# Kernel optimization log

Measured on AMD Instinct MI355X. Metric: run time of the kernel, lower is better.

Reference implementation:

```python
import jax, jax.numpy as jnp
import numpy as np

FEATURE_DIM = 512
NUM_HEADS = 8
HEAD_DIM = FEATURE_DIM // NUM_HEADS
B, L = 4, 2048


def setup_inputs() -> dict:
    key = jax.random.key(0)
    ks = jax.random.split(key, 10)
    s = 1.0 / np.sqrt(FEATURE_DIM)
    inp = {
        "ppg": jax.random.normal(ks[0], (B, FEATURE_DIM, L), dtype=jnp.float32),
        "ecg": jax.random.normal(ks[1], (B, FEATURE_DIM, L), dtype=jnp.float32),
        "Wq": jax.random.uniform(ks[2], (FEATURE_DIM, FEATURE_DIM), jnp.float32, -s, s),
        "bq": jnp.zeros((FEATURE_DIM,), jnp.float32),
        "Wk": jax.random.uniform(ks[3], (FEATURE_DIM, FEATURE_DIM), jnp.float32, -s, s),
        "bk": jnp.zeros((FEATURE_DIM,), jnp.float32),
        "Wv": jax.random.uniform(ks[4], (FEATURE_DIM, FEATURE_DIM), jnp.float32, -s, s),
        "bv": jnp.zeros((FEATURE_DIM,), jnp.float32),
        "Wo": jax.random.uniform(ks[5], (FEATURE_DIM, FEATURE_DIM), jnp.float32, -s, s),
        "bo": jnp.zeros((FEATURE_DIM,), jnp.float32),
    }
    return inp


def reference(ppg, ecg, Wq, bq, Wk, bk, Wv, bv, Wo, bo):
    # ppg/ecg: (B, C, L) -> (B, L, C)
    x = jnp.transpose(ppg, (0, 2, 1))
    y = jnp.transpose(ecg, (0, 2, 1))
    q = x @ Wq.T + bq  # (B, L, C)
    k = y @ Wk.T + bk
    v = y @ Wv.T + bv
    # split heads: (B, H, L, D)
    def split(t):
        return jnp.transpose(t.reshape(B, L, NUM_HEADS, HEAD_DIM), (0, 2, 1, 3))
    qh, kh, vh = split(q), split(k), split(v)
    scores = jnp.einsum('bhqd,bhkd->bhqk', qh, kh) / jnp.sqrt(jnp.float32(HEAD_DIM))
    probs = jax.nn.softmax(scores, axis=-1)  # dropout is identity in eval mode
    ctx = jnp.einsum('bhqk,bhkd->bhqd', probs, vh)
    ctx = jnp.transpose(ctx, (0, 2, 1, 3)).reshape(B, L, FEATURE_DIM)
    out = ctx @ Wo.T + bo + x  # residual with transposed ppg
    return jnp.transpose(out, (0, 2, 1))  # (B, C, L)
```

## Files before the change

kernel.cpp:

```cpp
#include <hip/hip_runtime.h>
#include <hip/hip_bf16.h>

static constexpr int Bc = 4;
static constexpr int Lc = 2048;
static constexpr int Cc = 512;
static constexpr int Hc = 8;
static constexpr int Dc = 64;

using short8  = __attribute__((ext_vector_type(8))) short;
using float4v = __attribute__((ext_vector_type(4))) float;

static __device__ __forceinline__ unsigned short f2bf(float f) {
    __hip_bfloat16 h = __float2bfloat16(f);
    return *reinterpret_cast<unsigned short*>(&h);
}

__global__ __launch_bounds__(256) void prep_kernel(
    const float* __restrict__ ppg, const float* __restrict__ ecg,
    const float* __restrict__ Wq, const float* __restrict__ Wk,
    const float* __restrict__ Wv, const float* __restrict__ Wo,
    unsigned short* __restrict__ Xt_ppg, unsigned short* __restrict__ Xt_ecg,
    unsigned short* __restrict__ Wbf)
{
    __shared__ float Ts[64 * 69];
    const int task = blockIdx.x;
    const int tid  = threadIdx.x;

    if (task < 2048) {
        const int src = task >> 10;
        const int rem = task & 1023;
        const int b   = rem >> 8;
        const int c0  = ((rem >> 5) & 7) * 64;
        const int l0  = (rem & 31) * 64;
        const float* X = src ? ecg : ppg;
        unsigned short* Xt = src ? Xt_ecg : Xt_ppg;

        #pragma unroll
        for (int j = 0; j < 4; ++j) {
            int idx = tid + j * 256;
            int c = idx >> 4, l4 = idx & 15;
            float4 v = *(const float4*)(X + ((size_t)b * Cc + c0 + c) * Lc + l0 + l4 * 4);
            Ts[c * 69 + l4 * 4 + 0] = v.x;
            Ts[c * 69 + l4 * 4 + 1] = v.y;
            Ts[c * 69 + l4 * 4 + 2] = v.z;
            Ts[c * 69 + l4 * 4 + 3] = v.w;
        }
        __syncthreads();
        #pragma unroll
        for (int j = 0; j < 8; ++j) {
            int u = tid + j * 256;
            int l = u >> 5, p2 = u & 31;
            float a = Ts[(2 * p2) * 69 + l];
            float bb = Ts[(2 * p2 + 1) * 69 + l];
            ushort2 pk; pk.x = f2bf(a); pk.y = f2bf(bb);
            *(ushort2*)(Xt + ((size_t)b * Lc + l0 + l) * Cc + c0 + 2 * p2) = pk;
        }
    } else {
        const int wb   = task - 2048;
        const int widx = wb >> 7;
        const float* W = widx == 0 ? Wq : widx == 1 ? Wk : widx == 2 ? Wv : Wo;
        size_t off = (size_t)(wb & 127) * 2048 + (size_t)tid * 8;
        float4 v0 = *(const float4*)(W + off);
        float4 v1 = *(const float4*)(W + off + 4);
        unsigned short pk[8] = {f2bf(v0.x), f2bf(v0.y), f2bf(v0.z), f2bf(v0.w),
                                f2bf(v1.x), f2bf(v1.y), f2bf(v1.z), f2bf(v1.w)};
        *(short8*)(Wbf + (size_t)widx * Cc * Cc + off) = *(const short8*)pk;
    }
}

__global__ __launch_bounds__(256) void proj_kernel(
    const unsigned short* __restrict__ Xt_ppg,
    const unsigned short* __restrict__ Xt_ecg,
    const unsigned short* __restrict__ Wbf,
    const float* __restrict__ bq, const float* __restrict__ bk,
    const float* __restrict__ bv,
    unsigned short* __restrict__ Qw, unsigned short* __restrict__ Kw,
    unsigned short* __restrict__ Vtw)
{
    constexpr int LDW = 72;
    const int z = blockIdx.z, p = z >> 2, b = z & 3;
    const int l0 = blockIdx.x * 64, n0 = blockIdx.y * 64;
    const unsigned short* X = (p == 0) ? Xt_ppg : Xt_ecg;
    const unsigned short* W = Wbf + (size_t)p * Cc * Cc;
    const float* bias = (p == 0) ? bq : (p == 1) ? bk : bv;

    const int tid = threadIdx.x, wave = tid >> 6, lane = tid & 63;
    const int l16 = lane & 15, quad = lane >> 4;

    __shared__ __align__(16) unsigned short At[64 * LDW];
    __shared__ __align__(16) unsigned short Bt[64 * LDW];

    float4v acc[4] = {};

    for (int c0 = 0; c0 < Cc; c0 += 64) {
        #pragma unroll
        for (int j = 0; j < 2; ++j) {
            int e = tid + j * 256;
            int row = e >> 3, c8 = e & 7;
            *(short8*)&At[row * LDW + c8 * 8] =
                *(const short8*)(X + ((size_t)b * Lc + l0 + row) * Cc + c0 + c8 * 8);
            *(short8*)&Bt[row * LDW + c8 * 8] =
                *(const short8*)(W + (size_t)(n0 + row) * Cc + c0 + c8 * 8);
        }
        __syncthreads();

        if (p < 2) {
            #pragma unroll
            for (int ks = 0; ks < 2; ++ks) {
                short8 af = *(const short8*)&At[(wave * 16 + l16) * LDW + ks * 32 + quad * 8];
                #pragma unroll
                for (int t = 0; t < 4; ++t) {
                    short8 bf = *(const short8*)&Bt[(t * 16 + l16) * LDW + ks * 32 + quad * 8];
                    acc[t] = __builtin_amdgcn_mfma_f32_16x16x32_bf16(af, bf, acc[t], 0, 0, 0);
                }
            }
        } else {
            #pragma unroll
            for (int ks = 0; ks < 2; ++ks) {
                short8 af = *(const short8*)&Bt[(wave * 16 + l16) * LDW + ks * 32 + quad * 8];
                #pragma unroll
                for (int t = 0; t < 4; ++t) {
                    short8 bf = *(const short8*)&At[(t * 16 + l16) * LDW + ks * 32 + quad * 8];
                    acc[t] = __builtin_amdgcn_mfma_f32_16x16x32_bf16(af, bf, acc[t], 0, 0, 0);
                }
            }
        }
        __syncthreads();
    }

    const int h = n0 >> 6;
    const int bh = b * Hc + h;

    if (p < 2) {
        const float sc = (p == 0) ? 0.18033688011112042f : 1.0f;
        unsigned short* dst = (p == 0) ? Qw : Kw;
        #pragma unroll
        for (int t = 0; t < 4; ++t) {
            float bia = bias[n0 + t * 16 + l16];
            #pragma unroll
            for (int r = 0; r < 4; ++r) {
                int l = l0 + wave * 16 + quad * 4 + r;
                dst[((size_t)bh * Lc + l) * Dc + t * 16 + l16] =
                    f2bf((acc[t][r] + bia) * sc);
            }
        }
    } else {
        #pragma unroll
        for (int t = 0; t < 4; ++t) {
            #pragma unroll
            for (int r = 0; r < 4; ++r) {
                int d = wave * 16 + quad * 4 + r;
                float bia = bias[n0 + d];
                int l = l0 + t * 16 + l16;
                Vtw[((size_t)bh * Dc + d) * Lc + l] = f2bf(acc[t][r] + bia);
            }
        }
    }
}

__global__ __launch_bounds__(256) void attn_mfma_kernel(
    const unsigned short* __restrict__ Qg,
    const unsigned short* __restrict__ Kg,
    const unsigned short* __restrict__ Vtg,
    unsigned short* __restrict__ ctx)
{
    constexpr int LDW = 72;
    const int bh   = blockIdx.y;
    const int q0   = blockIdx.x * 128;
    const int tid  = threadIdx.x;
    const int wave = tid >> 6;
    const int lane = tid & 63;
    const int l16  = lane & 15;
    const int quad = lane >> 4;

    __shared__ __align__(16) unsigned short Kt[64 * LDW];
    __shared__ __align__(16) unsigned short Vt[64 * LDW];
    __shared__ __align__(16) unsigned short PT[128 * LDW];

    const unsigned short* Qb = Qg + ((size_t)bh * Lc + q0) * Dc;
    #pragma unroll
    for (int j = 0; j < 4; ++j) {
        int e = tid + j * 256;
        int row = e >> 3, c8 = e & 7;
        *(short8*)&PT[row * LDW + c8 * 8] =
            *(const short8*)(Qb + row * Dc + c8 * 8);
    }
    __syncthreads();

    short8 qf[2][2];
    #pragma unroll
    for (int qt = 0; qt < 2; ++qt)
        #pragma unroll
        for (int ks = 0; ks < 2; ++ks)
            qf[qt][ks] = *(const short8*)&PT[(wave * 32 + qt * 16 + l16) * LDW
                                             + ks * 32 + quad * 8];

    float4v O[4][2] = {};
    float lsum[2] = {0.0f, 0.0f};

    for (int kc = 0; kc < Lc; kc += 64) {
        __syncthreads();
        const unsigned short* Kb = Kg + ((size_t)bh * Lc + kc) * Dc;
        const unsigned short* Vb = Vtg + (size_t)bh * (Dc * Lc) + kc;
        #pragma unroll
        for (int j = 0; j < 2; ++j) {
            int e = tid + j * 256;
            int row = e >> 3, c8 = e & 7;
            *(short8*)&Kt[row * LDW + c8 * 8] =
                *(const short8*)(Kb + row * Dc + c8 * 8);
            *(short8*)&Vt[row * LDW + c8 * 8] =
                *(const short8*)(Vb + (size_t)row * Lc + c8 * 8);
        }
        __syncthreads();

        float4v S[4][2];
        #pragma unroll
        for (int kt = 0; kt < 4; ++kt)
            #pragma unroll
            for (int qt = 0; qt < 2; ++qt)
                S[kt][qt] = (float4v){0.f, 0.f, 0.f, 0.f};
        #pragma unroll
        for (int ks = 0; ks < 2; ++ks) {
            #pragma unroll
            for (int kt = 0; kt < 4; ++kt) {
                short8 af = *(const short8*)&Kt[(kt * 16 + l16) * LDW
                                                + ks * 32 + quad * 8];
                #pragma unroll
                for (int qt = 0; qt < 2; ++qt)
                    S[kt][qt] = __builtin_amdgcn_mfma_f32_16x16x32_bf16(
                        af, qf[qt][ks], S[kt][qt], 0, 0, 0);
            }
        }

        #pragma unroll
        for (int qt = 0; qt < 2; ++qt) {
            float ls = 0.0f;
            #pragma unroll
            for (int kt = 0; kt < 4; ++kt) {
                float p0 = __builtin_amdgcn_exp2f(S[kt][qt][0]);
                float p1 = __builtin_amdgcn_exp2f(S[kt][qt][1]);
                float p2 = __builtin_amdgcn_exp2f(S[kt][qt][2]);
                float p3 = __builtin_amdgcn_exp2f(S[kt][qt][3]);
                ls += (p0 + p1) + (p2 + p3);
                ushort4 pk;
                pk.x = f2bf(p0); pk.y = f2bf(p1); pk.z = f2bf(p2); pk.w = f2bf(p3);
                *(ushort4*)&PT[(wave * 32 + qt * 16 + l16) * LDW
                               + kt * 16 + quad * 4] = pk;
            }
            lsum[qt] += ls;
        }

        #pragma unroll
        for (int ks = 0; ks < 2; ++ks) {
            short8 pf[2];
            #pragma unroll
            for (int qt = 0; qt < 2; ++qt)
                pf[qt] = *(const short8*)&PT[(wave * 32 + qt * 16 + l16) * LDW
                                             + ks * 32 + quad * 8];
            #pragma unroll
            for (int dt = 0; dt < 4; ++dt) {
                short8 vf = *(const short8*)&Vt[(dt * 16 + l16) * LDW
                                                + ks * 32 + quad * 8];
                #pragma unroll
                for (int qt = 0; qt < 2; ++qt)
                    O[dt][qt] = __builtin_amdgcn_mfma_f32_16x16x32_bf16(
                        vf, pf[qt], O[dt][qt], 0, 0, 0);
            }
        }
    }

    float inv_l[2];
    #pragma unroll
    for (int qt = 0; qt < 2; ++qt) {
        float t = lsum[qt];
        t += __shfl_xor(t, 16, 64);
        t += __shfl_xor(t, 32, 64);
        inv_l[qt] = 1.0f / t;
    }
    const int b = bh >> 3, h = bh & 7;
    #pragma unroll
    for (int dt = 0; dt < 4; ++dt) {
        #pragma unroll
        for (int qt = 0; qt < 2; ++qt) {
            int q = q0 + wave * 32 + qt * 16 + l16;
            ushort4 pk;
            pk.x = f2bf(O[dt][qt][0] * inv_l[qt]);
            pk.y = f2bf(O[dt][qt][1] * inv_l[qt]);
            pk.z = f2bf(O[dt][qt][2] * inv_l[qt]);
            pk.w = f2bf(O[dt][qt][3] * inv_l[qt]);
            *(ushort4*)(ctx + ((size_t)b * Lc + q) * Cc
                        + h * Dc + dt * 16 + quad * 4) = pk;
        }
    }
}

__global__ __launch_bounds__(256) void outproj_kernel(
    const unsigned short* __restrict__ ctx, const unsigned short* __restrict__ Wo_bf,
    const float* __restrict__ bo, const float* __restrict__ ppg,
    float* __restrict__ out)
{
    constexpr int LDW = 72;
    const int b = blockIdx.z;
    const int l0 = blockIdx.x * 64, n0 = blockIdx.y * 64;
    const int tid = threadIdx.x, wave = tid >> 6, lane = tid & 63;
    const int l16 = lane & 15, quad = lane >> 4;

    __shared__ __align__(16) unsigned short At[64 * LDW];
    __shared__ __align__(16) unsigned short Bt[64 * LDW];

    float4v acc[4] = {};

    for (int c0 = 0; c0 < Cc; c0 += 64) {
        #pragma unroll
        for (int j = 0; j < 2; ++j) {
            int e = tid + j * 256;
            int row = e >> 3, c8 = e & 7;
            *(short8*)&At[row * LDW + c8 * 8] =
                *(const short8*)(Wo_bf + (size_t)(n0 + row) * Cc + c0 + c8 * 8);
            *(short8*)&Bt[row * LDW + c8 * 8] =
                *(const short8*)(ctx + ((size_t)b * Lc + l0 + row) * Cc + c0 + c8 * 8);
        }
        __syncthreads();

        #pragma unroll
        for (int ks = 0; ks < 2; ++ks) {
            short8 af = *(const short8*)&At[(wave * 16 + l16) * LDW + ks * 32 + quad * 8];
            #pragma unroll
            for (int t = 0; t < 4; ++t) {
                short8 bf = *(const short8*)&Bt[(t * 16 + l16) * LDW + ks * 32 + quad * 8];
                acc[t] = __builtin_amdgcn_mfma_f32_16x16x32_bf16(af, bf, acc[t], 0, 0, 0);
            }
        }
        __syncthreads();
    }

    #pragma unroll
    for (int t = 0; t < 4; ++t) {
        #pragma unroll
        for (int r = 0; r < 4; ++r) {
            int n = n0 + wave * 16 + quad * 4 + r;
            int l = l0 + t * 16 + l16;
            size_t oidx = ((size_t)b * Cc + n) * Lc + l;
            out[oidx] = acc[t][r] + bo[n] + ppg[oidx];
        }
    }
}

extern "C" void kernel_launch(void* const* d_in, const int* in_sizes, int n_in,
                              void* d_out, int out_size, void* d_ws, size_t ws_size,
                              hipStream_t stream) {
    const float* ppg = (const float*)d_in[0];
    const float* ecg = (const float*)d_in[1];
    const float* Wq  = (const float*)d_in[2];
    const float* bq  = (const float*)d_in[3];
    const float* Wk  = (const float*)d_in[4];
    const float* bk  = (const float*)d_in[5];
    const float* Wv  = (const float*)d_in[6];
    const float* bv  = (const float*)d_in[7];
    const float* Wo  = (const float*)d_in[8];
    const float* bo  = (const float*)d_in[9];
    float* out = (float*)d_out;

    const size_t plane = (size_t)Bc * Lc * Cc;
    unsigned short* Xt_ppg = (unsigned short*)d_ws;
    unsigned short* Xt_ecg = Xt_ppg + plane;
    unsigned short* Wbf    = Xt_ecg + plane;
    unsigned short* Qw     = Wbf + (size_t)4 * Cc * Cc;
    unsigned short* Kw     = Qw + plane;
    unsigned short* Vtw    = Kw + plane;
    unsigned short* ctx    = Vtw + plane;

    prep_kernel<<<2560, 256, 0, stream>>>(ppg, ecg, Wq, Wk, Wv, Wo,
                                          Xt_ppg, Xt_ecg, Wbf);

    dim3 g1(Lc / 64, Cc / 64, 3 * Bc);
    proj_kernel<<<g1, 256, 0, stream>>>(Xt_ppg, Xt_ecg, Wbf, bq, bk, bv,
                                        Qw, Kw, Vtw);

    dim3 g2(Lc / 128, Bc * Hc);
    attn_mfma_kernel<<<g2, 256, 0, stream>>>(Qw, Kw, Vtw, ctx);

    dim3 g3(Lc / 64, Cc / 64, Bc);
    outproj_kernel<<<g3, 256, 0, stream>>>(ctx, Wbf + (size_t)3 * Cc * Cc,
                                           bo, ppg, out);
}
```

Baseline: 211.4 us.

## Register-prefetch next tiles in projection and attention, retile both kernels

Both the projection GEMM and the attention kernel now load the next K-chunk (or K/V tile) from global memory into registers while the current tile is being consumed from shared memory, overlapping load latency with MFMA work. The projection kernel doubles its L tile to 128 rows, so each block reuses the weight tile across more rows. The attention kernel halves its query tile to 64 rows, giving twice as many blocks for more occupancy and parallelism, at the cost of re-reading K/V more often. Register pressure rises, and an extra barrier per iteration is added in attention.

```diff
diff --git a/kernel.cpp b/kernel.cpp
--- a/kernel.cpp
+++ b/kernel.cpp
@@ -79,7 +79,7 @@
 {
     constexpr int LDW = 72;
     const int z = blockIdx.z, p = z >> 2, b = z & 3;
-    const int l0 = blockIdx.x * 64, n0 = blockIdx.y * 64;
+    const int l0 = blockIdx.x * 128, n0 = blockIdx.y * 64;
     const unsigned short* X = (p == 0) ? Xt_ppg : Xt_ecg;
     const unsigned short* W = Wbf + (size_t)p * Cc * Cc;
     const float* bias = (p == 0) ? bq : (p == 1) ? bk : bv;
@@ -87,41 +87,67 @@
     const int tid = threadIdx.x, wave = tid >> 6, lane = tid & 63;
     const int l16 = lane & 15, quad = lane >> 4;
 
-    __shared__ __align__(16) unsigned short At[64 * LDW];
+    __shared__ __align__(16) unsigned short At[128 * LDW];
     __shared__ __align__(16) unsigned short Bt[64 * LDW];
 
-    float4v acc[4] = {};
+    float4v acc[8] = {};
+    short8 areg[4], breg[2];
+
+    const int arow = tid >> 3, ac8 = tid & 7;
+    #pragma unroll
+    for (int j = 0; j < 4; ++j)
+        areg[j] = *(const short8*)(X + ((size_t)b * Lc + l0 + arow + j * 32) * Cc + ac8 * 8);
+    #pragma unroll
+    for (int j = 0; j < 2; ++j)
+        breg[j] = *(const short8*)(W + (size_t)(n0 + arow + j * 32) * Cc + ac8 * 8);
 
     for (int c0 = 0; c0 < Cc; c0 += 64) {
         #pragma unroll
-        for (int j = 0; j < 2; ++j) {
-            int e = tid + j * 256;
-            int row = e >> 3, c8 = e & 7;
-            *(short8*)&At[row * LDW + c8 * 8] =
-                *(const short8*)(X + ((size_t)b * Lc + l0 + row) * Cc + c0 + c8 * 8);
-            *(short8*)&Bt[row * LDW + c8 * 8] =
-                *(const short8*)(W + (size_t)(n0 + row) * Cc + c0 + c8 * 8);
-        }
-        __syncthreads();
+        for (int j = 0; j < 4; ++j)
+            *(short8*)&At[(arow + j * 32) * LDW + ac8 * 8] = areg[j];
+        #pragma unroll
+        for (int j = 0; j < 2; ++j)
+            *(short8*)&Bt[(arow + j * 32) * LDW + ac8 * 8] = breg[j];
+        __syncthreads();
+
+        if (c0 + 64 < Cc) {
+            #pragma unroll
+            for (int j = 0; j < 4; ++j)
+                areg[j] = *(const short8*)(X + ((size_t)b * Lc + l0 + arow + j * 32) * Cc
+                                           + c0 + 64 + ac8 * 8);
+            #pragma unroll
+            for (int j = 0; j < 2; ++j)
+                breg[j] = *(const short8*)(W + (size_t)(n0 + arow + j * 32) * Cc
+                                           + c0 + 64 + ac8 * 8);
+        }
 
         if (p < 2) {
             #pragma unroll
             for (int ks = 0; ks < 2; ++ks) {
-                short8 af = *(const short8*)&At[(wave * 16 + l16) * LDW + ks * 32 + quad * 8];
                 #pragma unroll
-                for (int t = 0; t < 4; ++t) {
-                    short8 bf = *(const short8*)&Bt[(t * 16 + l16) * LDW + ks * 32 + quad * 8];
-                    acc[t] = __builtin_amdgcn_mfma_f32_16x16x32_bf16(af, bf, acc[t], 0, 0, 0);
+                for (int lt = 0; lt < 2; ++lt) {
+                    short8 af = *(const short8*)&At[(wave * 32 + lt * 16 + l16) * LDW
+                                                    + ks * 32 + quad * 8];
+                    #pragma unroll
+                    for (int t = 0; t < 4; ++t) {
+                        short8 bf = *(const short8*)&Bt[(t * 16 + l16) * LDW
+                                                        + ks * 32 + quad * 8];
+                        acc[lt * 4 + t] = __builtin_amdgcn_mfma_f32_16x16x32_bf16(
+                            af, bf, acc[lt * 4 + t], 0, 0, 0);
+                    }
                 }
             }
         } else {
             #pragma unroll
             for (int ks = 0; ks < 2; ++ks) {
-                short8 af = *(const short8*)&Bt[(wave * 16 + l16) * LDW + ks * 32 + quad * 8];
+                short8 af = *(const short8*)&Bt[(wave * 16 + l16) * LDW
+                                                + ks * 32 + quad * 8];
                 #pragma unroll
-                for (int t = 0; t < 4; ++t) {
-                    short8 bf = *(const short8*)&At[(t * 16 + l16) * LDW + ks * 32 + quad * 8];
-                    acc[t] = __builtin_amdgcn_mfma_f32_16x16x32_bf16(af, bf, acc[t], 0, 0, 0);
+                for (int t = 0; t < 8; ++t) {
+                    short8 bf = *(const short8*)&At[(t * 16 + l16) * LDW
+                                                    + ks * 32 + quad * 8];
+                    acc[t] = __builtin_amdgcn_mfma_f32_16x16x32_bf16(
+                        af, bf, acc[t], 0, 0, 0);
                 }
             }
         }
@@ -135,18 +161,21 @@
         const float sc = (p == 0) ? 0.18033688011112042f : 1.0f;
         unsigned short* dst = (p == 0) ? Qw : Kw;
         #pragma unroll
-        for (int t = 0; t < 4; ++t) {
-            float bia = bias[n0 + t * 16 + l16];
-            #pragma unroll
-            for (int r = 0; r < 4; ++r) {
-                int l = l0 + wave * 16 + quad * 4 + r;
-                dst[((size_t)bh * Lc + l) * Dc + t * 16 + l16] =
-                    f2bf((acc[t][r] + bia) * sc);
+        for (int lt = 0; lt < 2; ++lt) {
+            #pragma unroll
+            for (int t = 0; t < 4; ++t) {
+                float bia = bias[n0 + t * 16 + l16];
+                #pragma unroll
+                for (int r = 0; r < 4; ++r) {
+                    int l = l0 + wave * 32 + lt * 16 + quad * 4 + r;
+                    dst[((size_t)bh * Lc + l) * Dc + t * 16 + l16] =
+                        f2bf((acc[lt * 4 + t][r] + bia) * sc);
+                }
             }
         }
     } else {
         #pragma unroll
-        for (int t = 0; t < 4; ++t) {
+        for (int t = 0; t < 8; ++t) {
             #pragma unroll
             for (int r = 0; r < 4; ++r) {
                 int d = wave * 16 + quad * 4 + r;
@@ -166,7 +195,7 @@
 {
     constexpr int LDW = 72;
     const int bh   = blockIdx.y;
-    const int q0   = blockIdx.x * 128;
+    const int q0   = blockIdx.x * 64;
     const int tid  = threadIdx.x;
     const int wave = tid >> 6;
     const int lane = tid & 63;
@@ -175,122 +204,110 @@
 
     __shared__ __align__(16) unsigned short Kt[64 * LDW];
     __shared__ __align__(16) unsigned short Vt[64 * LDW];
-    __shared__ __align__(16) unsigned short PT[128 * LDW];
+    __shared__ __align__(16) unsigned short PT[64 * LDW];
+
+    const int srow = tid >> 3, sc8 = tid & 7;
 
     const unsigned short* Qb = Qg + ((size_t)bh * Lc + q0) * Dc;
     #pragma unroll
-    for (int j = 0; j < 4; ++j) {
-        int e = tid + j * 256;
-        int row = e >> 3, c8 = e & 7;
-        *(short8*)&PT[row * LDW + c8 * 8] =
-            *(const short8*)(Qb + row * Dc + c8 * 8);
-    }
+    for (int j = 0; j < 2; ++j)
+        *(short8*)&PT[(srow + j * 32) * LDW + sc8 * 8] =
+            *(const short8*)(Qb + (srow + j * 32) * Dc + sc8 * 8);
     __syncthreads();
 
-    short8 qf[2][2];
-    #pragma unroll
-    for (int qt = 0; qt < 2; ++qt)
-        #pragma unroll
-        for (int ks = 0; ks < 2; ++ks)
-            qf[qt][ks] = *(const short8*)&PT[(wave * 32 + qt * 16 + l16) * LDW
-                                             + ks * 32 + quad * 8];
-
-    float4v O[4][2] = {};
-    float lsum[2] = {0.0f, 0.0f};
+    short8 qf[2];
+    #pragma unroll
+    for (int ks = 0; ks < 2; ++ks)
+        qf[ks] = *(const short8*)&PT[(wave * 16 + l16) * LDW + ks * 32 + quad * 8];
+
+    float4v O[4] = {};
+    float lsum = 0.0f;
+
+    const unsigned short* Kb0 = Kg + (size_t)bh * Lc * Dc;
+    const unsigned short* Vb0 = Vtg + (size_t)bh * (Dc * Lc);
+
+    short8 kreg[2], vreg[2];
+    #pragma unroll
+    for (int j = 0; j < 2; ++j) {
+        kreg[j] = *(const short8*)(Kb0 + (size_t)(srow + j * 32) * Dc + sc8 * 8);
+        vreg[j] = *(const short8*)(Vb0 + (size_t)(srow + j * 32) * Lc + sc8 * 8);
+    }
 
     for (int kc = 0; kc < Lc; kc += 64) {
-        __syncthreads();
-        const unsigned short* Kb = Kg + ((size_t)bh * Lc + kc) * Dc;
-        const unsigned short* Vb = Vtg + (size_t)bh * (Dc * Lc) + kc;
         #pragma unroll
         for (int j = 0; j < 2; ++j) {
-            int e = tid + j * 256;
-            int row = e >> 3, c8 = e & 7;
-            *(short8*)&Kt[row * LDW + c8 * 8] =
-                *(const short8*)(Kb + row * Dc + c8 * 8);
-            *(short8*)&Vt[row * LDW + c8 * 8] =
-                *(const short8*)(Vb + (size_t)row * Lc + c8 * 8);
-        }
-        __syncthreads();
-
-        float4v S[4][2];
-        #pragma unroll
-        for (int kt = 0; kt < 4; ++kt)
-            #pragma unroll
-            for (int qt = 0; qt < 2; ++qt)
-                S[kt][qt] = (float4v){0.f, 0.f, 0.f, 0.f};
+            *(short8*)&Kt[(srow + j * 32) * LDW + sc8 * 8] = kreg[j];
+            *(short8*)&Vt[(srow + j * 32) * LDW + sc8 * 8] = vreg[j];
+        }
+        __syncthreads();
+
+        if (kc + 64 < Lc) {
+            #pragma unroll
+            for (int j = 0; j < 2; ++j) {
+                kreg[j] = *(const short8*)(Kb0 + (size_t)(kc + 64 + srow + j * 32) * Dc
+                                           + sc8 * 8);
+                vreg[j] = *(const short8*)(Vb0 + (size_t)(srow + j * 32) * Lc
+                                           + kc + 64 + sc8 * 8);
+            }
+        }
+
+        float4v S[4];
+        #pragma unroll
+        for (int kt = 0; kt < 4; ++kt) S[kt] = (float4v){0.f, 0.f, 0.f, 0.f};
         #pragma unroll
         for (int ks = 0; ks < 2; ++ks) {
             #pragma unroll
             for (int kt = 0; kt < 4; ++kt) {
                 short8 af = *(const short8*)&Kt[(kt * 16 + l16) * LDW
                                                 + ks * 32 + quad * 8];
-                #pragma unroll
-                for (int qt = 0; qt < 2; ++qt)
-                    S[kt][qt] = __builtin_amdgcn_mfma_f32_16x16x32_bf16(
-                        af, qf[qt][ks], S[kt][qt], 0, 0, 0);
-            }
-        }
-
-        #pragma unroll
-        for (int qt = 0; qt < 2; ++qt) {
-            float ls = 0.0f;
-            #pragma unroll
-            for (int kt = 0; kt < 4; ++kt) {
-                float p0 = __builtin_amdgcn_exp2f(S[kt][qt][0]);
-                float p1 = __builtin_amdgcn_exp2f(S[kt][qt][1]);
-                float p2 = __builtin_amdgcn_exp2f(S[kt][qt][2]);
-                float p3 = __builtin_amdgcn_exp2f(S[kt][qt][3]);
-                ls += (p0 + p1) + (p2 + p3);
-                ushort4 pk;
-                pk.x = f2bf(p0); pk.y = f2bf(p1); pk.z = f2bf(p2); pk.w = f2bf(p3);
-                *(ushort4*)&PT[(wave * 32 + qt * 16 + l16) * LDW
-                               + kt * 16 + quad * 4] = pk;
-            }
-            lsum[qt] += ls;
+                S[kt] = __builtin_amdgcn_mfma_f32_16x16x32_bf16(
+                    af, qf[ks], S[kt], 0, 0, 0);
+            }
+        }
+
+        #pragma unroll
+        for (int kt = 0; kt < 4; ++kt) {
+            float p0 = __builtin_amdgcn_exp2f(S[kt][0]);
+            float p1 = __builtin_amdgcn_exp2f(S[kt][1]);
+            float p2 = __builtin_amdgcn_exp2f(S[kt][2]);
+            float p3 = __builtin_amdgcn_exp2f(S[kt][3]);
+            lsum += (p0 + p1) + (p2 + p3);
+            ushort4 pk;
+            pk.x = f2bf(p0); pk.y = f2bf(p1); pk.z = f2bf(p2); pk.w = f2bf(p3);
+            *(ushort4*)&PT[(wave * 16 + l16) * LDW + kt * 16 + quad * 4] = pk;
         }
 
         #pragma unroll
         for (int ks = 0; ks < 2; ++ks) {
-            short8 pf[2];
-            #pragma unroll
-            for (int qt = 0; qt < 2; ++qt)
-                pf[qt] = *(const short8*)&PT[(wave * 32 + qt * 16 + l16) * LDW
-                                             + ks * 32 + quad * 8];
+            short8 pf = *(const short8*)&PT[(wave * 16 + l16) * LDW
+                                            + ks * 32 + quad * 8];
             #pragma unroll
             for (int dt = 0; dt < 4; ++dt) {
                 short8 vf = *(const short8*)&Vt[(dt * 16 + l16) * LDW
                                                 + ks * 32 + quad * 8];
-                #pragma unroll
-                for (int qt = 0; qt < 2; ++qt)
-                    O[dt][qt] = __builtin_amdgcn_mfma_f32_16x16x32_bf16(
-                        vf, pf[qt], O[dt][qt], 0, 0, 0);
-            }
-        }
-    }
-
-    float inv_l[2];
-    #pragma unroll
-    for (int qt = 0; qt < 2; ++qt) {
-        float t = lsum[qt];
-        t += __shfl_xor(t, 16, 64);
-        t += __shfl_xor(t, 32, 64);
-        inv_l[qt] = 1.0f / t;
-    }
+                O[dt] = __builtin_amdgcn_mfma_f32_16x16x32_bf16(
+                    vf, pf, O[dt], 0, 0, 0);
+            }
+        }
+        __syncthreads();
+    }
+
+    float t = lsum;
+    t += __shfl_xor(t, 16, 64);
+    t += __shfl_xor(t, 32, 64);
+    const float inv_l = 1.0f / t;
+
     const int b = bh >> 3, h = bh & 7;
+    const int q = q0 + wave * 16 + l16;
     #pragma unroll
     for (int dt = 0; dt < 4; ++dt) {
-        #pragma unroll
-        for (int qt = 0; qt < 2; ++qt) {
-            int q = q0 + wave * 32 + qt * 16 + l16;
-            ushort4 pk;
-            pk.x = f2bf(O[dt][qt][0] * inv_l[qt]);
-            pk.y = f2bf(O[dt][qt][1] * inv_l[qt]);
-            pk.z = f2bf(O[dt][qt][2] * inv_l[qt]);
-            pk.w = f2bf(O[dt][qt][3] * inv_l[qt]);
-            *(ushort4*)(ctx + ((size_t)b * Lc + q) * Cc
-                        + h * Dc + dt * 16 + quad * 4) = pk;
-        }
+        ushort4 pk;
+        pk.x = f2bf(O[dt][0] * inv_l);
+        pk.y = f2bf(O[dt][1] * inv_l);
+        pk.z = f2bf(O[dt][2] * inv_l);
+        pk.w = f2bf(O[dt][3] * inv_l);
+        *(ushort4*)(ctx + ((size_t)b * Lc + q) * Cc
+                    + h * Dc + dt * 16 + quad * 4) = pk;
     }
 }
 
@@ -373,11 +390,11 @@
     prep_kernel<<<2560, 256, 0, stream>>>(ppg, ecg, Wq, Wk, Wv, Wo,
                                           Xt_ppg, Xt_ecg, Wbf);
 
-    dim3 g1(Lc / 64, Cc / 64, 3 * Bc);
+    dim3 g1(Lc / 128, Cc / 64, 3 * Bc);
     proj_kernel<<<g1, 256, 0, stream>>>(Xt_ppg, Xt_ecg, Wbf, bq, bk, bv,
                                         Qw, Kw, Vtw);
 
-    dim3 g2(Lc / 128, Bc * Hc);
+    dim3 g2(Lc / 64, Bc * Hc);
     attn_mfma_kernel<<<g2, 256, 0, stream>>>(Qw, Kw, Vtw, ctx);
 
     dim3 g3(Lc / 64, Cc / 64, Bc);
```

Result: faster. 194.1 us (-8.2%).
